# Kernel optimization log

Hardware: AMD Instinct MI355X
Metric: run time of the kernel (lower is better)

Reference implementation:

```python
import jax, jax.numpy as jnp
import numpy as np
import math

B, T, D, H, L, V = 2, 1024, 768, 12, 4, 50257
HD = D // H
ROPE_PCT = 0.5
MAX_WL = 10000.0
EPS = 1e-5


def setup_inputs() -> dict:
    key = jax.random.key(0)
    ks = jax.random.split(key, 8)
    s = 0.02
    return {
        "idx": jax.random.randint(ks[0], (B, T), 0, V, dtype=jnp.int32),
        "wte": jax.random.normal(ks[1], (V, D), jnp.float32) * s,
        "ln1_g": jnp.ones((L, D), jnp.float32),
        "ln1_b": jnp.zeros((L, D), jnp.float32),
        "Wqkv": jax.random.normal(ks[2], (L, D, 3 * D), jnp.float32) * s,
        "bqkv": jnp.zeros((L, 3 * D), jnp.float32),
        "Wo": jax.random.normal(ks[3], (L, D, D), jnp.float32) * s,
        "bo": jnp.zeros((L, D), jnp.float32),
        "ln2_g": jnp.ones((L, D), jnp.float32),
        "ln2_b": jnp.zeros((L, D), jnp.float32),
        "Wfc": jax.random.normal(ks[4], (L, D, 4 * D), jnp.float32) * s,
        "bfc": jnp.zeros((L, 4 * D), jnp.float32),
        "Wp": jax.random.normal(ks[5], (L, 4 * D, D), jnp.float32) * s,
        "bp": jnp.zeros((L, D), jnp.float32),
        "lnf_g": jnp.ones((D,), jnp.float32),
        "lnf_b": jnp.zeros((D,), jnp.float32),
        "Wlm": jax.random.normal(ks[6], (D, V), jnp.float32) * s,
    }


def _ln(x, g, b):
    m = x.mean(-1, keepdims=True)
    v = x.var(-1, keepdims=True)
    return (x - m) / jnp.sqrt(v + EPS) * g + b


def _gelu(x):
    return 0.5 * x * (1.0 + jnp.tanh(math.sqrt(2.0 / math.pi) * (x + 0.044715 * x ** 3)))


def _p_rope(x, positions):
    # x: [B, H, T, HD]; partial RoPE: rotate first ROPE_PCT of angle pairs, leave rest.
    rope_angles = int(ROPE_PCT * HD // 2)
    nope_angles = HD // 2 - rope_angles
    fraction = 2.0 * jnp.arange(0, rope_angles) / HD
    timescale = jnp.power(MAX_WL, fraction)
    timescale = jnp.pad(timescale, (0, nope_angles), constant_values=jnp.inf)
    sinusoid = positions[:, None] / timescale[None, :]  # [T, HD//2]; pos/inf = 0 -> no rotation
    sin, cos = jnp.sin(sinusoid), jnp.cos(sinusoid)
    first, second = jnp.split(x, 2, axis=-1)
    out = jnp.concatenate([first * cos - second * sin, second * cos + first * sin], axis=-1)
    return out.astype(x.dtype)


def reference(idx, wte, ln1_g, ln1_b, Wqkv, bqkv, Wo, bo, ln2_g, ln2_b, Wfc, bfc, Wp, bp, lnf_g, lnf_b, Wlm):
    x = wte[idx]  # [B, T, D]
    positions = jnp.arange(T, dtype=x.dtype)
    causal = jnp.tril(jnp.ones((T, T), dtype=bool))
    scale = jnp.sqrt(jnp.float32(HD)).astype(x.dtype)
    for l in range(L):
        h1 = _ln(x, ln1_g[l], ln1_b[l])
        h2 = _ln(x, ln2_g[l], ln2_b[l])  # note: both LNs read the same x (as in source)
        # attention
        qkv = h1 @ Wqkv[l] + bqkv[l]
        q, k, v = jnp.split(qkv, 3, axis=-1)
        sh = lambda t: t.reshape(B, T, H, HD).transpose(0, 2, 1, 3)
        q, k, v = sh(q), sh(k), sh(v)
        q = _p_rope(q, positions)
        k = _p_rope(k, positions)
        att = jnp.einsum('bhqd,bhkd->bhqk', q, k) / scale
        att = jnp.where(causal, att, jnp.finfo(att.dtype).min)
        att = jax.nn.softmax(att, axis=-1)
        y = jnp.einsum('bhqk,bhkd->bhqd', att, v)
        y = y.transpose(0, 2, 1, 3).reshape(B, T, D)
        x = x + (y @ Wo[l] + bo[l])
        # MLP
        h = _gelu(h2 @ Wfc[l] + bfc[l])
        x = x + (h @ Wp[l] + bp[l])
    x = _ln(x, lnf_g, lnf_b)
    logits = x @ Wlm  # [B, T, V]
    return logits
```

## Files before the change

### kernel.cpp

```cpp
#include <hip/hip_runtime.h>

typedef unsigned short u16;
typedef unsigned int u32;
typedef __attribute__((ext_vector_type(8))) short bf16x8;
typedef __attribute__((ext_vector_type(4))) float f32x4;

#define SEQ 1024
#define DM 768
#define NH 12
#define HD2 64
#define NLAYER 4
#define NVOCAB 50257
#define BT 2048

__device__ __forceinline__ u16 f2bf(float f) {
  union { float f; u32 u; } v; v.f = f;
  u32 r = v.u + 0x7FFFu + ((v.u >> 16) & 1u);
  return (u16)(r >> 16);
}
__device__ __forceinline__ float bf2f(u16 u) {
  union { u32 u; float f; } v; v.u = ((u32)u) << 16;
  return v.f;
}

__device__ __forceinline__ void glds16(const u16* g, u16* l) {
  __builtin_amdgcn_global_load_lds(
      (const __attribute__((address_space(1))) u32*)(const void*)g,
      (__attribute__((address_space(3))) u32*)(void*)l, 16, 0, 0);
}

__global__ void k_embed(const int* __restrict__ idx, const float* __restrict__ wte,
                        float* __restrict__ xf) {
  int r = blockIdx.x;
  int tok = idx[r];
  const float* s = wte + (size_t)tok * DM;
  float* d = xf + (size_t)r * DM;
  for (int c = threadIdx.x; c < DM; c += 256) d[c] = s[c];
}

__global__ void k_trig(float* __restrict__ ctab, float* __restrict__ stab) {
  int gid = blockIdx.x * 256 + threadIdx.x;
  int tt = gid >> 4, j = gid & 15;
  float inv = powf(10000.f, -(float)j * (1.f / 32.f));
  float ang = (float)tt * inv;
  ctab[gid] = cosf(ang);
  stab[gid] = sinf(ang);
}

__global__ void k_cvtT(const float* __restrict__ in, u16* __restrict__ out,
                       int R, int C) {
  __shared__ u16 t[64][68];
  int c0 = blockIdx.x * 64, r0 = blockIdx.y * 64;
  int tx = threadIdx.x & 15, ty = threadIdx.x >> 4;
  int c = c0 + tx * 4;
#pragma unroll
  for (int i = 0; i < 4; ++i) {
    int r = r0 + ty + i * 16;
    float4 v = make_float4(0.f, 0.f, 0.f, 0.f);
    if (c + 3 < C) {
      v = *(const float4*)&in[(size_t)r * C + c];
    } else {
      if (c + 0 < C) v.x = in[(size_t)r * C + c];
      if (c + 1 < C) v.y = in[(size_t)r * C + c + 1];
      if (c + 2 < C) v.z = in[(size_t)r * C + c + 2];
      if (c + 3 < C) v.w = in[(size_t)r * C + c + 3];
    }
    t[ty + i * 16][tx * 4 + 0] = f2bf(v.x);
    t[ty + i * 16][tx * 4 + 1] = f2bf(v.y);
    t[ty + i * 16][tx * 4 + 2] = f2bf(v.z);
    t[ty + i * 16][tx * 4 + 3] = f2bf(v.w);
  }
  __syncthreads();
  int wl = threadIdx.x & 31, grp = threadIdx.x >> 5;
#pragma unroll
  for (int it = 0; it < 8; ++it) {
    int cc = it * 8 + grp;
    int gcol = c0 + cc;
    if (gcol < C) {
      u32 wv = (u32)t[2 * wl][cc] | ((u32)t[2 * wl + 1][cc] << 16);
      *(u32*)&out[(size_t)gcol * R + r0 + 2 * wl] = wv;
    }
  }
}

__device__ __forceinline__ float bsum(float v, float* red) {
#pragma unroll
  for (int o = 32; o > 0; o >>= 1) v += __shfl_down(v, o);
  if ((threadIdx.x & 63) == 0) red[threadIdx.x >> 6] = v;
  __syncthreads();
  if (threadIdx.x == 0) red[4] = red[0] + red[1] + red[2] + red[3];
  __syncthreads();
  return red[4];
}

__global__ void k_ln(const float* __restrict__ x, const float* __restrict__ g1,
                     const float* __restrict__ b1, const float* __restrict__ g2,
                     const float* __restrict__ b2, u16* __restrict__ o1,
                     u16* __restrict__ o2) {
  __shared__ float red[8];
  int r = blockIdx.x;
  int t = threadIdx.x;
  const float* xr = x + (size_t)r * DM;
  float v0 = xr[t], v1 = xr[t + 256], v2 = xr[t + 512];
  float mean = bsum(v0 + v1 + v2, red) * (1.f / DM);
  float d0 = v0 - mean, d1 = v1 - mean, d2 = v2 - mean;
  float var = bsum(d0 * d0 + d1 * d1 + d2 * d2, red) * (1.f / DM);
  float rstd = rsqrtf(var + 1e-5f);
  u16* p1 = o1 + (size_t)r * DM;
  p1[t]       = f2bf(d0 * rstd * g1[t]       + b1[t]);
  p1[t + 256] = f2bf(d1 * rstd * g1[t + 256] + b1[t + 256]);
  p1[t + 512] = f2bf(d2 * rstd * g1[t + 512] + b1[t + 512]);
  if (o2) {
    u16* p2 = o2 + (size_t)r * DM;
    p2[t]       = f2bf(d0 * rstd * g2[t]       + b2[t]);
    p2[t + 256] = f2bf(d1 * rstd * g2[t + 256] + b2[t + 256]);
    p2[t + 512] = f2bf(d2 * rstd * g2[t + 512] + b2[t + 512]);
  }
}

__global__ void k_attn(const u16* __restrict__ qr, const u16* __restrict__ kr,
                       const u16* __restrict__ vT, u16* __restrict__ yb) {
  int ti = (int)gridDim.x - 1 - (int)blockIdx.x;
  int bh = blockIdx.y;
  __shared__ u16 Ps[64 * 72];
  __shared__ u16 Ks[2][4096];
  __shared__ u16 Vs[2][4096];
  int tid = threadIdx.x;
  int rr = tid >> 2, cc = tid & 3;
  int w = tid >> 6, l = tid & 63;
  int rl = l & 15, g = l >> 4;
  {
    const u16* gq = qr + ((size_t)bh * SEQ + ti * 64 + rr) * HD2;
    *(uint4*)&Ps[rr * 72 + cc * 8]      = *(const uint4*)(gq + cc * 8);
    *(uint4*)&Ps[rr * 72 + cc * 8 + 32] = *(const uint4*)(gq + cc * 8 + 32);
  }
  int srow = w * 8 + (l >> 3);
  int gs = (l & 7) ^ (l >> 3);
  const u16* gkb = kr + (size_t)bh * SEQ * HD2;
  const u16* gvb = vT + (size_t)bh * HD2 * SEQ;
  glds16(gkb + (size_t)srow * 64 + gs * 8,        &Ks[0][w * 512]);
  glds16(gkb + (size_t)(32 + srow) * 64 + gs * 8, &Ks[0][2048 + w * 512]);
  glds16(gvb + (size_t)srow * SEQ + gs * 8,       &Vs[0][w * 512]);
  glds16(gvb + (size_t)(32 + srow) * SEQ + gs * 8,&Vs[0][2048 + w * 512]);
  __syncthreads();
  bf16x8 aq0 = *(const bf16x8*)&Ps[(w * 16 + rl) * 72 + g * 8];
  bf16x8 aq1 = *(const bf16x8*)&Ps[(w * 16 + rl) * 72 + 32 + g * 8];
  float m[4], lsum[4];
  f32x4 oacc[4] = {};
#pragma unroll
  for (int r2 = 0; r2 < 4; ++r2) { m[r2] = -3.0e38f; lsum[r2] = 0.f; }
  int qloc = w * 16 + g * 4;
  int sw = rl & 7;
  int cur = 0;
  for (int kt = 0; kt <= ti; ++kt) {
    if (kt < ti) {
      int nx = cur ^ 1;
      glds16(gkb + (size_t)((kt + 1) * 64 + srow) * 64 + gs * 8,      &Ks[nx][w * 512]);
      glds16(gkb + (size_t)((kt + 1) * 64 + 32 + srow) * 64 + gs * 8, &Ks[nx][2048 + w * 512]);
      glds16(gvb + (size_t)srow * SEQ + (kt + 1) * 64 + gs * 8,       &Vs[nx][w * 512]);
      glds16(gvb + (size_t)(32 + srow) * SEQ + (kt + 1) * 64 + gs * 8,&Vs[nx][2048 + w * 512]);
    }
    f32x4 s[4] = {};
    __builtin_amdgcn_s_setprio(1);
#pragma unroll
    for (int nt = 0; nt < 4; ++nt) {
      int r = (nt * 16 + rl) * 64;
      bf16x8 b0 = *(const bf16x8*)&Ks[cur][r + ((0 + g) ^ sw) * 8];
      bf16x8 b1 = *(const bf16x8*)&Ks[cur][r + ((4 + g) ^ sw) * 8];
      s[nt] = __builtin_amdgcn_mfma_f32_16x16x32_bf16(aq0, b0, s[nt], 0, 0, 0);
      s[nt] = __builtin_amdgcn_mfma_f32_16x16x32_bf16(aq1, b1, s[nt], 0, 0, 0);
    }
    __builtin_amdgcn_s_setprio(0);
#pragma unroll
    for (int nt = 0; nt < 4; ++nt) s[nt] *= 0.125f;
    if (kt == ti) {
#pragma unroll
      for (int nt = 0; nt < 4; ++nt) {
        int col = nt * 16 + rl;
#pragma unroll
        for (int r2 = 0; r2 < 4; ++r2)
          if (col > qloc + r2) s[nt][r2] = -3.0e38f;
      }
    }
#pragma unroll
    for (int r2 = 0; r2 < 4; ++r2) {
      float pm = fmaxf(fmaxf(s[0][r2], s[1][r2]), fmaxf(s[2][r2], s[3][r2]));
#pragma unroll
      for (int o = 1; o < 16; o <<= 1) pm = fmaxf(pm, __shfl_xor(pm, o));
      float mn = fmaxf(m[r2], pm);
      float corr = __expf(m[r2] - mn);
      float p0 = __expf(s[0][r2] - mn);
      float p1 = __expf(s[1][r2] - mn);
      float p2 = __expf(s[2][r2] - mn);
      float p3 = __expf(s[3][r2] - mn);
      float ps = p0 + p1 + p2 + p3;
#pragma unroll
      for (int o = 1; o < 16; o <<= 1) ps += __shfl_xor(ps, o);
      lsum[r2] = lsum[r2] * corr + ps;
      m[r2] = mn;
      oacc[0][r2] *= corr; oacc[1][r2] *= corr;
      oacc[2][r2] *= corr; oacc[3][r2] *= corr;
      int prow = (qloc + r2) * 72;
      Ps[prow + rl]      = f2bf(p0);
      Ps[prow + 16 + rl] = f2bf(p1);
      Ps[prow + 32 + rl] = f2bf(p2);
      Ps[prow + 48 + rl] = f2bf(p3);
    }
    bf16x8 pa0 = *(const bf16x8*)&Ps[(w * 16 + rl) * 72 + g * 8];
    bf16x8 pa1 = *(const bf16x8*)&Ps[(w * 16 + rl) * 72 + 32 + g * 8];
    __builtin_amdgcn_s_setprio(1);
#pragma unroll
    for (int nt = 0; nt < 4; ++nt) {
      int r = (nt * 16 + rl) * 64;
      bf16x8 b0 = *(const bf16x8*)&Vs[cur][r + ((0 + g) ^ sw) * 8];
      bf16x8 b1 = *(const bf16x8*)&Vs[cur][r + ((4 + g) ^ sw) * 8];
      oacc[nt] = __builtin_amdgcn_mfma_f32_16x16x32_bf16(pa0, b0, oacc[nt], 0, 0, 0);
      oacc[nt] = __builtin_amdgcn_mfma_f32_16x16x32_bf16(pa1, b1, oacc[nt], 0, 0, 0);
    }
    __builtin_amdgcn_s_setprio(0);
    __syncthreads();
    cur ^= 1;
  }
  int b = bh / NH, h = bh % NH;
  float invl[4];
#pragma unroll
  for (int r2 = 0; r2 < 4; ++r2) invl[r2] = 1.f / lsum[r2];
#pragma unroll
  for (int nt = 0; nt < 4; ++nt) {
    int d = nt * 16 + rl;
#pragma unroll
    for (int r2 = 0; r2 < 4; ++r2) {
      int trow = ti * 64 + qloc + r2;
      yb[((size_t)(b * SEQ + trow)) * DM + h * HD2 + d] = f2bf(oacc[nt][r2] * invl[r2]);
    }
  }
}

template <int MODE>
__global__ void k_g128(const u16* __restrict__ A, const u16* __restrict__ Bt,
                       const float* __restrict__ bias, u16* __restrict__ outb,
                       float* __restrict__ outf, int M, int N, int K, int MT,
                       const float* __restrict__ ctab,
                       const float* __restrict__ stab, u16* __restrict__ qrp,
                       u16* __restrict__ krp, u16* __restrict__ vTp) {
  __shared__ u16 SM[16384];
  float* cw = (float*)SM;
  int nwg = gridDim.x;
  int id = blockIdx.x;
  if ((nwg & 7) == 0) id = (id & 7) * (nwg >> 3) + (id >> 3);
  int mt = id % MT, nt = id / MT;
  int m0 = mt * 128, n0 = nt * 128;
  int tid = threadIdx.x;
  int w = tid >> 6, l = tid & 63;
  int srow = w * 16 + (l >> 2);
  int gs = (l & 3) ^ ((l >> 3) & 3);
  const u16* gA0 = A + (size_t)(m0 + srow) * K + gs * 8;
  const u16* gA1 = A + (size_t)(m0 + 64 + srow) * K + gs * 8;
  int rb0 = n0 + srow;      if (rb0 > N - 1) rb0 = N - 1;
  int rb1 = n0 + 64 + srow; if (rb1 > N - 1) rb1 = N - 1;
  const u16* gB0 = Bt + (size_t)rb0 * K + gs * 8;
  const u16* gB1 = Bt + (size_t)rb1 * K + gs * 8;
  int wm = (w >> 1) * 64, wn = (w & 1) * 64;
  int rl = l & 15, g = l >> 4;
  int sla = g ^ ((rl >> 1) & 3);
  f32x4 acc[4][4] = {};
  int nK = K >> 5;
  int cur = 0;
  {
    u16* dA = SM + w * 512;
    glds16(gA0, dA); glds16(gA1, dA + 2048);
    u16* dB = SM + 4096 + w * 512;
    glds16(gB0, dB); glds16(gB1, dB + 2048);
  }
  __syncthreads();
  for (int kt = 0; kt < nK; ++kt) {
    if (kt + 1 < nK) {
      u16* dA = SM + (cur ^ 1) * 8192 + w * 512;
      glds16(gA0 + (kt + 1) * 32, dA); glds16(gA1 + (kt + 1) * 32, dA + 2048);
      u16* dB = dA + 4096;
      glds16(gB0 + (kt + 1) * 32, dB); glds16(gB1 + (kt + 1) * 32, dB + 2048);
    }
    const u16* As = SM + cur * 8192;
    const u16* Bs = As + 4096;
    bf16x8 af[4], bfr[4];
    __builtin_amdgcn_s_setprio(1);
#pragma unroll
    for (int i = 0; i < 4; ++i)
      af[i] = *(const bf16x8*)&As[(wm + i * 16 + rl) * 32 + sla * 8];
#pragma unroll
    for (int j = 0; j < 4; ++j)
      bfr[j] = *(const bf16x8*)&Bs[(wn + j * 16 + rl) * 32 + sla * 8];
#pragma unroll
    for (int i = 0; i < 4; ++i)
#pragma unroll
      for (int j = 0; j < 4; ++j)
        acc[i][j] = __builtin_amdgcn_mfma_f32_16x16x32_bf16(af[i], bfr[j],
                                                            acc[i][j], 0, 0, 0);
    __builtin_amdgcn_s_setprio(0);
    __syncthreads();
    cur ^= 1;
  }
  int reg = n0 / DM;
  int h0 = (n0 % DM) / 64;
  int bb = m0 >> 10;
  int t0 = m0 & (SEQ - 1);
  size_t bhbase = (size_t)bb * NH;
#pragma unroll
  for (int ch = 0; ch < 4; ++ch) {
    if ((w >> 1) == (ch >> 1)) {
      int ib = (ch & 1) * 2;
#pragma unroll
      for (int ii = 0; ii < 2; ++ii) {
#pragma unroll
        for (int j = 0; j < 4; ++j) {
          int col = wn + j * 16 + rl;
#pragma unroll
          for (int r2 = 0; r2 < 4; ++r2) {
            int rowc = ii * 16 + g * 4 + r2;
            float v = acc[ib + ii][j][r2];
            if (MODE != 3) {
              v += bias[n0 + col];
              if (MODE == 1) {
                float u = 0.7978845608028654f * (v + 0.044715f * v * v * v);
                v = 0.5f * v * (1.f + tanhf(u));
              }
            }
            cw[rowc * 132 + col] = v;
          }
        }
      }
    }
    __syncthreads();
    if (MODE == 3) {
      for (int t = tid; t < 4096; t += 256) {
        int rowc = t >> 7, col = t & 127;
        int gc = n0 + col;
        if (gc < N)
          __builtin_nontemporal_store(cw[rowc * 132 + col],
                                      &outf[(size_t)(m0 + ch * 32 + rowc) * N + gc]);
      }
    } else if (MODE == 1) {
      for (int t = tid; t < 2048; t += 256) {
        int rowc = t >> 6, cp = t & 63;
        u32 wv = (u32)f2bf(cw[rowc * 132 + 2 * cp]) |
                 ((u32)f2bf(cw[rowc * 132 + 2 * cp + 1]) << 16);
        *(u32*)&outb[(size_t)(m0 + ch * 32 + rowc) * N + n0 + 2 * cp] = wv;
      }
    } else {
      if (reg < 2) {
        u16* dst = (reg == 0) ? qrp : krp;
        for (int t = tid; t < 2048; t += 256) {
          int rowc = t >> 6, cp = t & 63;
          int c = 2 * cp;
          int hh = c >> 6, d = c & 63;
          int tt = t0 + ch * 32 + rowc;
          float x0 = cw[rowc * 132 + c];
          float x1 = cw[rowc * 132 + c + 1];
          float o0, o1;
          if (d < 32) {
            float y0 = cw[rowc * 132 + c + 32];
            float y1 = cw[rowc * 132 + c + 33];
            float c0 = 1.f, s0 = 0.f, c1 = 1.f, s1 = 0.f;
            if (d < 16) {
              c0 = ctab[tt * 16 + d];     s0 = stab[tt * 16 + d];
              c1 = ctab[tt * 16 + d + 1]; s1 = stab[tt * 16 + d + 1];
            }
            o0 = x0 * c0 - y0 * s0;
            o1 = x1 * c1 - y1 * s1;
          } else {
            int j = d - 32;
            float y0 = cw[rowc * 132 + c - 32];
            float y1 = cw[rowc * 132 + c - 31];
            float c0 = 1.f, s0 = 0.f, c1 = 1.f, s1 = 0.f;
            if (j < 16) {
              c0 = ctab[tt * 16 + j];     s0 = stab[tt * 16 + j];
              c1 = ctab[tt * 16 + j + 1]; s1 = stab[tt * 16 + j + 1];
            }
            o0 = x0 * c0 + y0 * s0;
            o1 = x1 * c1 + y1 * s1;
          }
          u32 wv = (u32)f2bf(o0) | ((u32)f2bf(o1) << 16);
          *(u32*)&dst[((bhbase + h0 + hh) * SEQ + tt) * HD2 + d] = wv;
        }
      } else {
        for (int t = tid; t < 2048; t += 256) {
          int dcol = t >> 4, p = t & 15;
          int hh = dcol >> 6, d = dcol & 63;
          int tt = t0 + ch * 32 + 2 * p;
          u32 wv = (u32)f2bf(cw[(2 * p) * 132 + dcol]) |
                   ((u32)f2bf(cw[(2 * p + 1) * 132 + dcol]) << 16);
          *(u32*)&vTp[((bhbase + h0 + hh) * HD2 + d) * SEQ + tt] = wv;
        }
      }
    }
    __syncthreads();
  }
}

__global__ void k_gemm64(const u16* __restrict__ A, const u16* __restrict__ Bt,
                         const float* __restrict__ bias,
                         float* __restrict__ outf, int M, int N, int K, int MT) {
  __shared__ u16 As[8192];
  __shared__ u16 Bs[8192];
  int nwg = gridDim.x;
  int id = blockIdx.x;
  if ((nwg & 7) == 0) id = (id & 7) * (nwg >> 3) + (id >> 3);
  int mt = id % MT, nt = id / MT;
  int sk = blockIdx.y, nsk = gridDim.y;
  int Kc = K / nsk, k0 = sk * Kc;
  int m0 = mt * 64, n0 = nt * 64;
  int tid = threadIdx.x;
  int w = tid >> 6, l = tid & 63;
  int row0 = tid >> 3, slot0 = tid & 7;
  int gs0 = slot0 ^ (row0 & 7);
  const u16* gA0 = A + (size_t)(m0 + row0) * K + k0 + gs0 * 8;
  const u16* gA1 = gA0 + (size_t)32 * K;
  const u16* gB0 = Bt + (size_t)(n0 + row0) * K + k0 + gs0 * 8;
  const u16* gB1 = gB0 + (size_t)32 * K;
  int wm = (w >> 1) * 32, wn = (w & 1) * 32;
  int rl = l & 15, g = l >> 4;
  int sl0 = g ^ (rl & 7), sl1 = (4 + g) ^ (rl & 7);
  f32x4 acc[2][2] = {};
  int nK = Kc >> 6;
  int cur = 0;
  {
    glds16(gA0, As + w * 512); glds16(gA1, As + 2048 + w * 512);
    glds16(gB0, Bs + w * 512); glds16(gB1, Bs + 2048 + w * 512);
  }
  __syncthreads();
  for (int kt = 0; kt < nK; ++kt) {
    if (kt + 1 < nK) {
      int nx = (cur ^ 1) * 4096;
      glds16(gA0 + (kt + 1) * 64, As + nx + w * 512);
      glds16(gA1 + (kt + 1) * 64, As + nx + 2048 + w * 512);
      glds16(gB0 + (kt + 1) * 64, Bs + nx + w * 512);
      glds16(gB1 + (kt + 1) * 64, Bs + nx + 2048 + w * 512);
    }
    const u16* Ac = As + cur * 4096;
    const u16* Bc = Bs + cur * 4096;
    bf16x8 a0[2], a1[2], b0[2], b1[2];
    __builtin_amdgcn_s_setprio(1);
#pragma unroll
    for (int i = 0; i < 2; ++i) {
      int r = (wm + i * 16 + rl) * 64;
      a0[i] = *(const bf16x8*)&Ac[r + sl0 * 8];
      a1[i] = *(const bf16x8*)&Ac[r + sl1 * 8];
    }
#pragma unroll
    for (int j = 0; j < 2; ++j) {
      int r = (wn + j * 16 + rl) * 64;
      b0[j] = *(const bf16x8*)&Bc[r + sl0 * 8];
      b1[j] = *(const bf16x8*)&Bc[r + sl1 * 8];
    }
#pragma unroll
    for (int i = 0; i < 2; ++i)
#pragma unroll
      for (int j = 0; j < 2; ++j) {
        acc[i][j] = __builtin_amdgcn_mfma_f32_16x16x32_bf16(a0[i], b0[j],
                                                            acc[i][j], 0, 0, 0);
        acc[i][j] = __builtin_amdgcn_mfma_f32_16x16x32_bf16(a1[i], b1[j],
                                                            acc[i][j], 0, 0, 0);
      }
    __builtin_amdgcn_s_setprio(0);
    __syncthreads();
    cur ^= 1;
  }
#pragma unroll
  for (int i = 0; i < 2; ++i) {
#pragma unroll
    for (int j = 0; j < 2; ++j) {
      int col = n0 + wn + j * 16 + rl;
      float bv = bias ? bias[col] : 0.f;
#pragma unroll
      for (int r2 = 0; r2 < 4; ++r2) {
        int row = m0 + wm + i * 16 + g * 4 + r2;
        float v = acc[i][j][r2];
        if (sk == 0) v += bv;
        atomicAdd(&outf[(size_t)row * N + col], v);
      }
    }
  }
}

__global__ void k_gemm_f32b(const u16* __restrict__ A, const float* __restrict__ B,
                            float* __restrict__ outf, int M, int N, int K) {
  __shared__ u16 As[128 * 40];
  __shared__ u16 Bs[4 * 128 * 12];
  int tid = threadIdx.x;
  int wid = tid >> 6, lane = tid & 63;
  int rl = lane & 15, g = lane >> 4;
  int m0 = blockIdx.x * 128, n0 = blockIdx.y * 128;
  int wm = (wid >> 1) * 64, wn = (wid & 1) * 64;
  int ar = tid >> 2, ac = tid & 3;
  int bn = tid & 127, bq = tid >> 7;
  f32x4 acc[4][4] = {};
  int nK = K / 32;
  for (int kt = 0; kt < nK; ++kt) {
    __syncthreads();
    {
      const u16* ga = A + (size_t)(m0 + ar) * K + kt * 32 + ac * 8;
      *(uint4*)&As[ar * 40 + ac * 8] = *(const uint4*)ga;
      *(uint4*)&As[(ar + 64) * 40 + ac * 8] = *(const uint4*)(ga + (size_t)64 * K);
    }
    int col = n0 + bn;
#pragma unroll
    for (int r = 0; r < 4; ++r) {
      int kq = bq + 2 * r;
      int kk = kt * 32 + kq * 4;
      float f0 = 0.f, f1 = 0.f, f2v = 0.f, f3 = 0.f;
      if (col < N) {
        const float* gb = B + (size_t)kk * N + col;
        f0 = gb[0]; f1 = gb[(size_t)N]; f2v = gb[(size_t)2 * N]; f3 = gb[(size_t)3 * N];
      }
      uint2 wv;
      wv.x = (u32)f2bf(f0) | ((u32)f2bf(f1) << 16);
      wv.y = (u32)f2bf(f2v) | ((u32)f2bf(f3) << 16);
      *(uint2*)&Bs[(kq >> 1) * 1536 + bn * 12 + (kq & 1) * 4] = wv;
    }
    __syncthreads();
    bf16x8 af[4], bfr[4];
#pragma unroll
    for (int mt = 0; mt < 4; ++mt)
      af[mt] = *(const bf16x8*)&As[(wm + mt * 16 + rl) * 40 + g * 8];
#pragma unroll
    for (int nt = 0; nt < 4; ++nt) {
      const u16* p = &Bs[g * 1536 + (wn + nt * 16 + rl) * 12];
      union { bf16x8 v; uint2 u2[2]; } tmp;
      tmp.u2[0] = *(const uint2*)p;
      tmp.u2[1] = *(const uint2*)(p + 4);
      bfr[nt] = tmp.v;
    }
#pragma unroll
    for (int mt = 0; mt < 4; ++mt)
#pragma unroll
      for (int nt = 0; nt < 4; ++nt)
        acc[mt][nt] = __builtin_amdgcn_mfma_f32_16x16x32_bf16(af[mt], bfr[nt],
                                                              acc[mt][nt], 0, 0, 0);
  }
#pragma unroll
  for (int mt = 0; mt < 4; ++mt)
#pragma unroll
    for (int nt = 0; nt < 4; ++nt) {
      int col = n0 + wn + nt * 16 + rl;
      if (col >= N) continue;
#pragma unroll
      for (int r2 = 0; r2 < 4; ++r2) {
        int row = m0 + wm + mt * 16 + g * 4 + r2;
        outf[(size_t)row * N + col] = acc[mt][nt][r2];
      }
    }
}

extern "C" void kernel_launch(void* const* d_in, const int* in_sizes, int n_in,
                              void* d_out, int out_size, void* d_ws, size_t ws_size,
                              hipStream_t stream) {
  (void)in_sizes; (void)n_in; (void)out_size;
  const int*   idx  = (const int*)  d_in[0];
  const float* wte  = (const float*)d_in[1];
  const float* ln1g = (const float*)d_in[2];
  const float* ln1b = (const float*)d_in[3];
  const float* Wqkv = (const float*)d_in[4];
  const float* bqkv = (const float*)d_in[5];
  const float* Wo   = (const float*)d_in[6];
  const float* bo   = (const float*)d_in[7];
  const float* ln2g = (const float*)d_in[8];
  const float* ln2b = (const float*)d_in[9];
  const float* Wfc  = (const float*)d_in[10];
  const float* bfc  = (const float*)d_in[11];
  const float* Wp   = (const float*)d_in[12];
  const float* bp   = (const float*)d_in[13];
  const float* lnfg = (const float*)d_in[14];
  const float* lnfb = (const float*)d_in[15];
  const float* Wlm  = (const float*)d_in[16];
  float* out = (float*)d_out;

  char* sb = (char*)d_out;
  size_t off = 0;
  auto alloc = [&](size_t bytes) {
    char* p = sb + off;
    off += (bytes + 255) & ~(size_t)255;
    return (void*)p;
  };
  float* xf  = (float*)alloc((size_t)BT * DM * 4);
  u16* h1b   = (u16*)alloc((size_t)BT * DM * 2);
  u16* h2b   = (u16*)alloc((size_t)BT * DM * 2);
  u16* qr    = (u16*)alloc((size_t)BT * DM * 2);
  u16* kr    = (u16*)alloc((size_t)BT * DM * 2);
  u16* vT    = (u16*)alloc((size_t)BT * DM * 2);
  u16* yb    = (u16*)alloc((size_t)BT * DM * 2);
  u16* hgel  = (u16*)alloc((size_t)BT * 4 * DM * 2);
  float* ctab = (float*)alloc((size_t)SEQ * 16 * 4);
  float* stab = (float*)alloc((size_t)SEQ * 16 * 4);
  u16* wqkvT = (u16*)alloc((size_t)NLAYER * 3 * DM * DM * 2);
  u16* woT   = (u16*)alloc((size_t)NLAYER * DM * DM * 2);
  u16* wfcT  = (u16*)alloc((size_t)NLAYER * 4 * DM * DM * 2);
  u16* wpT   = (u16*)alloc((size_t)NLAYER * 4 * DM * DM * 2);

  size_t wlmT_bytes = (size_t)NVOCAB * DM * 2;
  size_t xlnf_bytes = (size_t)BT * DM * 2;
  bool fast_lm = ws_size >= wlmT_bytes + xlnf_bytes + 512;
  u16* wlmT = (u16*)d_ws;
  u16* xlnf = fast_lm ? (u16*)((char*)d_ws + ((wlmT_bytes + 255) & ~(size_t)255))
                      : (u16*)d_ws;

  k_trig<<<(SEQ * 16) / 256, 256, 0, stream>>>(ctab, stab);
  for (int l = 0; l < NLAYER; ++l) {
    k_cvtT<<<dim3((3 * DM + 63) / 64, DM / 64), 256, 0, stream>>>(
        Wqkv + (size_t)l * DM * 3 * DM, wqkvT + (size_t)l * 3 * DM * DM, DM, 3 * DM);
    k_cvtT<<<dim3(DM / 64, DM / 64), 256, 0, stream>>>(
        Wo + (size_t)l * DM * DM, woT + (size_t)l * DM * DM, DM, DM);
    k_cvtT<<<dim3((4 * DM) / 64, DM / 64), 256, 0, stream>>>(
        Wfc + (size_t)l * DM * 4 * DM, wfcT + (size_t)l * 4 * DM * DM, DM, 4 * DM);
    k_cvtT<<<dim3(DM / 64, (4 * DM) / 64), 256, 0, stream>>>(
        Wp + (size_t)l * 4 * DM * DM, wpT + (size_t)l * 4 * DM * DM, 4 * DM, DM);
  }
  if (fast_lm)
    k_cvtT<<<dim3((NVOCAB + 63) / 64, DM / 64), 256, 0, stream>>>(Wlm, wlmT, DM, NVOCAB);

  k_embed<<<BT, 256, 0, stream>>>(idx, wte, xf);
  for (int l = 0; l < NLAYER; ++l) {
    k_ln<<<BT, 256, 0, stream>>>(xf, ln1g + l * DM, ln1b + l * DM,
                                 ln2g + l * DM, ln2b + l * DM, h1b, h2b);
    k_g128<4><<<(BT / 128) * (3 * DM / 128), 256, 0, stream>>>(
        h1b, wqkvT + (size_t)l * 3 * DM * DM, bqkv + (size_t)l * 3 * DM,
        nullptr, nullptr, BT, 3 * DM, DM, BT / 128, ctab, stab, qr, kr, vT);
    k_attn<<<dim3(SEQ / 64, 2 * NH), 256, 0, stream>>>(qr, kr, vT, yb);
    k_gemm64<<<dim3((BT / 64) * (DM / 64), 2), 256, 0, stream>>>(
        yb, woT + (size_t)l * DM * DM, bo + (size_t)l * DM, xf, BT, DM, DM, BT / 64);
    k_g128<1><<<(BT / 128) * (4 * DM / 128), 256, 0, stream>>>(
        h2b, wfcT + (size_t)l * 4 * DM * DM, bfc + (size_t)l * 4 * DM,
        hgel, nullptr, BT, 4 * DM, DM, BT / 128,
        nullptr, nullptr, nullptr, nullptr, nullptr);
    k_gemm64<<<dim3((BT / 64) * (DM / 64), 4), 256, 0, stream>>>(
        hgel, wpT + (size_t)l * 4 * DM * DM, bp + (size_t)l * DM, xf, BT, DM, 4 * DM,
        BT / 64);
  }
  k_ln<<<BT, 256, 0, stream>>>(xf, lnfg, lnfb, nullptr, nullptr, xlnf, nullptr);
  if (fast_lm) {
    int nt = (NVOCAB + 127) / 128;
    k_g128<3><<<(BT / 128) * nt, 256, 0, stream>>>(
        xlnf, wlmT, nullptr, nullptr, out, BT, NVOCAB, DM, BT / 128,
        nullptr, nullptr, nullptr, nullptr, nullptr);
  } else {
    k_gemm_f32b<<<dim3(BT / 128, (NVOCAB + 127) / 128), 256, 0, stream>>>(
        xlnf, Wlm, out, BT, NVOCAB, DM);
  }
}
```

Before: 1.057 ms.

## Add 64x128 GEMM kernel for QKV/FC, fold softmax scale into Q, lazy rescale

The QKV and FC projections move to a new 64x128-tile kernel with a BK=64 double-buffered LDS pipeline, giving twice as many workgroups, and k_g128 is cut down to the LM-head path only. The 1/sqrt(d) softmax scale is folded into Q during the RoPE epilogue, removing the per-tile multiply in attention. Attention also switches to a lazy max-rescale that only rescales the accumulators when the row max grows by more than 8, skipping many exp and multiply ops. The lazy threshold lets unnormalised probabilities reach about e^8, which stays safe in fp32 but slightly changes bf16 rounding of P.

```diff
diff --git a/kernel.cpp b/kernel.cpp
--- a/kernel.cpp
+++ b/kernel.cpp
@@ -171,8 +171,6 @@
       s[nt] = __builtin_amdgcn_mfma_f32_16x16x32_bf16(aq1, b1, s[nt], 0, 0, 0);
     }
     __builtin_amdgcn_s_setprio(0);
-#pragma unroll
-    for (int nt = 0; nt < 4; ++nt) s[nt] *= 0.125f;
     if (kt == ti) {
 #pragma unroll
       for (int nt = 0; nt < 4; ++nt) {
@@ -187,19 +185,21 @@
       float pm = fmaxf(fmaxf(s[0][r2], s[1][r2]), fmaxf(s[2][r2], s[3][r2]));
 #pragma unroll
       for (int o = 1; o < 16; o <<= 1) pm = fmaxf(pm, __shfl_xor(pm, o));
-      float mn = fmaxf(m[r2], pm);
-      float corr = __expf(m[r2] - mn);
-      float p0 = __expf(s[0][r2] - mn);
-      float p1 = __expf(s[1][r2] - mn);
-      float p2 = __expf(s[2][r2] - mn);
-      float p3 = __expf(s[3][r2] - mn);
+      if (pm > m[r2] + 8.f) {
+        float corr = __expf(m[r2] - pm);
+        m[r2] = pm;
+        lsum[r2] *= corr;
+        oacc[0][r2] *= corr; oacc[1][r2] *= corr;
+        oacc[2][r2] *= corr; oacc[3][r2] *= corr;
+      }
+      float p0 = __expf(s[0][r2] - m[r2]);
+      float p1 = __expf(s[1][r2] - m[r2]);
+      float p2 = __expf(s[2][r2] - m[r2]);
+      float p3 = __expf(s[3][r2] - m[r2]);
       float ps = p0 + p1 + p2 + p3;
 #pragma unroll
       for (int o = 1; o < 16; o <<= 1) ps += __shfl_xor(ps, o);
-      lsum[r2] = lsum[r2] * corr + ps;
-      m[r2] = mn;
-      oacc[0][r2] *= corr; oacc[1][r2] *= corr;
-      oacc[2][r2] *= corr; oacc[3][r2] *= corr;
+      lsum[r2] += ps;
       int prow = (qloc + r2) * 72;
       Ps[prow + rl]      = f2bf(p0);
       Ps[prow + 16 + rl] = f2bf(p1);
@@ -238,11 +238,7 @@
 
 template <int MODE>
 __global__ void k_g128(const u16* __restrict__ A, const u16* __restrict__ Bt,
-                       const float* __restrict__ bias, u16* __restrict__ outb,
-                       float* __restrict__ outf, int M, int N, int K, int MT,
-                       const float* __restrict__ ctab,
-                       const float* __restrict__ stab, u16* __restrict__ qrp,
-                       u16* __restrict__ krp, u16* __restrict__ vTp) {
+                       float* __restrict__ outf, int M, int N, int K, int MT) {
   __shared__ u16 SM[16384];
   float* cw = (float*)SM;
   int nwg = gridDim.x;
@@ -300,11 +296,6 @@
     __syncthreads();
     cur ^= 1;
   }
-  int reg = n0 / DM;
-  int h0 = (n0 % DM) / 64;
-  int bb = m0 >> 10;
-  int t0 = m0 & (SEQ - 1);
-  size_t bhbase = (size_t)bb * NH;
 #pragma unroll
   for (int ch = 0; ch < 4; ++ch) {
     if ((w >> 1) == (ch >> 1)) {
@@ -317,89 +308,182 @@
 #pragma unroll
           for (int r2 = 0; r2 < 4; ++r2) {
             int rowc = ii * 16 + g * 4 + r2;
-            float v = acc[ib + ii][j][r2];
-            if (MODE != 3) {
-              v += bias[n0 + col];
-              if (MODE == 1) {
-                float u = 0.7978845608028654f * (v + 0.044715f * v * v * v);
-                v = 0.5f * v * (1.f + tanhf(u));
-              }
-            }
-            cw[rowc * 132 + col] = v;
+            cw[rowc * 132 + col] = acc[ib + ii][j][r2];
           }
         }
       }
     }
     __syncthreads();
-    if (MODE == 3) {
+    for (int t = tid; t < 4096; t += 256) {
+      int rowc = t >> 7, col = t & 127;
+      int gc = n0 + col;
+      if (gc < N)
+        __builtin_nontemporal_store(cw[rowc * 132 + col],
+                                    &outf[(size_t)(m0 + ch * 32 + rowc) * N + gc]);
+    }
+    __syncthreads();
+  }
+}
+
+template <int MODE>
+__global__ void k_gw(const u16* __restrict__ A, const u16* __restrict__ Bt,
+                     const float* __restrict__ bias, u16* __restrict__ outb,
+                     int M, int N, int K, int MT,
+                     const float* __restrict__ ctab,
+                     const float* __restrict__ stab, u16* __restrict__ qrp,
+                     u16* __restrict__ krp, u16* __restrict__ vTp) {
+  __shared__ u16 SM2[24576];
+  float* cw = (float*)SM2;
+  int nwg = gridDim.x;
+  int id = blockIdx.x;
+  if ((nwg & 7) == 0) id = (id & 7) * (nwg >> 3) + (id >> 3);
+  int mt = id % MT, nt = id / MT;
+  int m0 = mt * 64, n0 = nt * 128;
+  int tid = threadIdx.x;
+  int w = tid >> 6, l = tid & 63;
+  int row0 = tid >> 3, slot0 = tid & 7;
+  int gs0 = slot0 ^ (row0 & 7);
+  const u16* gA0 = A + (size_t)(m0 + row0) * K + gs0 * 8;
+  const u16* gA1 = gA0 + (size_t)32 * K;
+  const u16* gB0 = Bt + (size_t)(n0 + row0) * K + gs0 * 8;
+  const u16* gB1 = gB0 + (size_t)32 * K;
+  const u16* gB2 = gB0 + (size_t)64 * K;
+  const u16* gB3 = gB0 + (size_t)96 * K;
+  int wm = (w >> 1) * 32, wn = (w & 1) * 64;
+  int rl = l & 15, g = l >> 4;
+  int sl0 = g ^ (rl & 7), sl1 = (4 + g) ^ (rl & 7);
+  f32x4 acc[2][4] = {};
+  int nK = K >> 6;
+  int cur = 0;
+  {
+    u16* dA = SM2;
+    glds16(gA0, dA + w * 512); glds16(gA1, dA + 2048 + w * 512);
+    u16* dB = SM2 + 8192;
+    glds16(gB0, dB + w * 512);        glds16(gB1, dB + 2048 + w * 512);
+    glds16(gB2, dB + 4096 + w * 512); glds16(gB3, dB + 6144 + w * 512);
+  }
+  __syncthreads();
+  for (int kt = 0; kt < nK; ++kt) {
+    if (kt + 1 < nK) {
+      int ka = (kt + 1) * 64;
+      u16* dA = SM2 + (cur ^ 1) * 4096;
+      glds16(gA0 + ka, dA + w * 512); glds16(gA1 + ka, dA + 2048 + w * 512);
+      u16* dB = SM2 + 8192 + (cur ^ 1) * 8192;
+      glds16(gB0 + ka, dB + w * 512);        glds16(gB1 + ka, dB + 2048 + w * 512);
+      glds16(gB2 + ka, dB + 4096 + w * 512); glds16(gB3 + ka, dB + 6144 + w * 512);
+    }
+    const u16* Ac = SM2 + cur * 4096;
+    const u16* Bc = SM2 + 8192 + cur * 8192;
+    bf16x8 a0[2], a1[2], b0[4], b1[4];
+    __builtin_amdgcn_s_setprio(1);
+#pragma unroll
+    for (int i = 0; i < 2; ++i) {
+      int r = (wm + i * 16 + rl) * 64;
+      a0[i] = *(const bf16x8*)&Ac[r + sl0 * 8];
+      a1[i] = *(const bf16x8*)&Ac[r + sl1 * 8];
+    }
+#pragma unroll
+    for (int j = 0; j < 4; ++j) {
+      int r = (wn + j * 16 + rl) * 64;
+      b0[j] = *(const bf16x8*)&Bc[r + sl0 * 8];
+      b1[j] = *(const bf16x8*)&Bc[r + sl1 * 8];
+    }
+#pragma unroll
+    for (int i = 0; i < 2; ++i)
+#pragma unroll
+      for (int j = 0; j < 4; ++j) {
+        acc[i][j] = __builtin_amdgcn_mfma_f32_16x16x32_bf16(a0[i], b0[j],
+                                                            acc[i][j], 0, 0, 0);
+        acc[i][j] = __builtin_amdgcn_mfma_f32_16x16x32_bf16(a1[i], b1[j],
+                                                            acc[i][j], 0, 0, 0);
+      }
+    __builtin_amdgcn_s_setprio(0);
+    __syncthreads();
+    cur ^= 1;
+  }
+#pragma unroll
+  for (int i = 0; i < 2; ++i) {
+#pragma unroll
+    for (int j = 0; j < 4; ++j) {
+      int col = wn + j * 16 + rl;
+      float bv = bias[n0 + col];
+#pragma unroll
+      for (int r2 = 0; r2 < 4; ++r2) {
+        float v = acc[i][j][r2] + bv;
+        if (MODE == 1) {
+          float u = 0.7978845608028654f * (v + 0.044715f * v * v * v);
+          v = 0.5f * v * (1.f + tanhf(u));
+        }
+        cw[(wm + i * 16 + g * 4 + r2) * 133 + col] = v;
+      }
+    }
+  }
+  __syncthreads();
+  if (MODE == 1) {
+    for (int t = tid; t < 4096; t += 256) {
+      int rowc = t >> 6, cp = t & 63;
+      u32 wv = (u32)f2bf(cw[rowc * 133 + 2 * cp]) |
+               ((u32)f2bf(cw[rowc * 133 + 2 * cp + 1]) << 16);
+      *(u32*)&outb[(size_t)(m0 + rowc) * N + n0 + 2 * cp] = wv;
+    }
+  } else {
+    int reg = n0 / DM;
+    int h0 = (n0 % DM) / 64;
+    int bb = m0 >> 10;
+    int t0 = m0 & (SEQ - 1);
+    size_t bhb = (size_t)bb * NH + h0;
+    if (reg < 2) {
+      u16* dst = (reg == 0) ? qrp : krp;
+      float qs = (reg == 0) ? 0.125f : 1.f;
       for (int t = tid; t < 4096; t += 256) {
-        int rowc = t >> 7, col = t & 127;
-        int gc = n0 + col;
-        if (gc < N)
-          __builtin_nontemporal_store(cw[rowc * 132 + col],
-                                      &outf[(size_t)(m0 + ch * 32 + rowc) * N + gc]);
-      }
-    } else if (MODE == 1) {
-      for (int t = tid; t < 2048; t += 256) {
         int rowc = t >> 6, cp = t & 63;
-        u32 wv = (u32)f2bf(cw[rowc * 132 + 2 * cp]) |
-                 ((u32)f2bf(cw[rowc * 132 + 2 * cp + 1]) << 16);
-        *(u32*)&outb[(size_t)(m0 + ch * 32 + rowc) * N + n0 + 2 * cp] = wv;
+        int c = 2 * cp;
+        int hh = c >> 6, d = c & 63;
+        int tt = t0 + rowc;
+        float x0 = cw[rowc * 133 + c];
+        float x1 = cw[rowc * 133 + c + 1];
+        float o0, o1;
+        if (d < 32) {
+          float y0 = cw[rowc * 133 + c + 32];
+          float y1 = cw[rowc * 133 + c + 33];
+          float c0 = 1.f, s0 = 0.f, c1 = 1.f, s1 = 0.f;
+          if (d < 16) {
+            c0 = ctab[tt * 16 + d];     s0 = stab[tt * 16 + d];
+            c1 = ctab[tt * 16 + d + 1]; s1 = stab[tt * 16 + d + 1];
+          }
+          o0 = x0 * c0 - y0 * s0;
+          o1 = x1 * c1 - y1 * s1;
+        } else {
+          int j = d - 32;
+          float y0 = cw[rowc * 133 + c - 32];
+          float y1 = cw[rowc * 133 + c - 31];
+          float c0 = 1.f, s0 = 0.f, c1 = 1.f, s1 = 0.f;
+          if (j < 16) {
+            c0 = ctab[tt * 16 + j];     s0 = stab[tt * 16 + j];
+            c1 = ctab[tt * 16 + j + 1]; s1 = stab[tt * 16 + j + 1];
+          }
+          o0 = x0 * c0 + y0 * s0;
+          o1 = x1 * c1 + y1 * s1;
+        }
+        u32 wv = (u32)f2bf(o0 * qs) | ((u32)f2bf(o1 * qs) << 16);
+        *(u32*)&dst[((bhb + hh) * SEQ + tt) * HD2 + d] = wv;
       }
     } else {
-      if (reg < 2) {
-        u16* dst = (reg == 0) ? qrp : krp;
-        for (int t = tid; t < 2048; t += 256) {
-          int rowc = t >> 6, cp = t & 63;
-          int c = 2 * cp;
-          int hh = c >> 6, d = c & 63;
-          int tt = t0 + ch * 32 + rowc;
-          float x0 = cw[rowc * 132 + c];
-          float x1 = cw[rowc * 132 + c + 1];
-          float o0, o1;
-          if (d < 32) {
-            float y0 = cw[rowc * 132 + c + 32];
-            float y1 = cw[rowc * 132 + c + 33];
-            float c0 = 1.f, s0 = 0.f, c1 = 1.f, s1 = 0.f;
-            if (d < 16) {
-              c0 = ctab[tt * 16 + d];     s0 = stab[tt * 16 + d];
-              c1 = ctab[tt * 16 + d + 1]; s1 = stab[tt * 16 + d + 1];
-            }
-            o0 = x0 * c0 - y0 * s0;
-            o1 = x1 * c1 - y1 * s1;
-          } else {
-            int j = d - 32;
-            float y0 = cw[rowc * 132 + c - 32];
-            float y1 = cw[rowc * 132 + c - 31];
-            float c0 = 1.f, s0 = 0.f, c1 = 1.f, s1 = 0.f;
-            if (j < 16) {
-              c0 = ctab[tt * 16 + j];     s0 = stab[tt * 16 + j];
-              c1 = ctab[tt * 16 + j + 1]; s1 = stab[tt * 16 + j + 1];
-            }
-            o0 = x0 * c0 + y0 * s0;
-            o1 = x1 * c1 + y1 * s1;
-          }
-          u32 wv = (u32)f2bf(o0) | ((u32)f2bf(o1) << 16);
-          *(u32*)&dst[((bhbase + h0 + hh) * SEQ + tt) * HD2 + d] = wv;
-        }
-      } else {
-        for (int t = tid; t < 2048; t += 256) {
-          int dcol = t >> 4, p = t & 15;
-          int hh = dcol >> 6, d = dcol & 63;
-          int tt = t0 + ch * 32 + 2 * p;
-          u32 wv = (u32)f2bf(cw[(2 * p) * 132 + dcol]) |
-                   ((u32)f2bf(cw[(2 * p + 1) * 132 + dcol]) << 16);
-          *(u32*)&vTp[((bhbase + h0 + hh) * HD2 + d) * SEQ + tt] = wv;
-        }
-      }
-    }
-    __syncthreads();
-  }
-}
-
-__global__ void k_gemm64(const u16* __restrict__ A, const u16* __restrict__ Bt,
-                         const float* __restrict__ bias,
-                         float* __restrict__ outf, int M, int N, int K, int MT) {
+      for (int t = tid; t < 4096; t += 256) {
+        int dcol = t >> 5, p = t & 31;
+        int hh = dcol >> 6, d = dcol & 63;
+        int tt = t0 + 2 * p;
+        u32 wv = (u32)f2bf(cw[(2 * p) * 133 + dcol]) |
+                 ((u32)f2bf(cw[(2 * p + 1) * 133 + dcol]) << 16);
+        *(u32*)&vTp[((bhb + hh) * HD2 + d) * SEQ + tt] = wv;
+      }
+    }
+  }
+}
+
+__global__ void k_g64r(const u16* __restrict__ A, const u16* __restrict__ Bt,
+                       const float* __restrict__ bias,
+                       float* __restrict__ outf, int M, int N, int K, int MT) {
   __shared__ u16 As[8192];
   __shared__ u16 Bs[8192];
   int nwg = gridDim.x;
@@ -621,17 +705,16 @@
   for (int l = 0; l < NLAYER; ++l) {
     k_ln<<<BT, 256, 0, stream>>>(xf, ln1g + l * DM, ln1b + l * DM,
                                  ln2g + l * DM, ln2b + l * DM, h1b, h2b);
-    k_g128<4><<<(BT / 128) * (3 * DM / 128), 256, 0, stream>>>(
+    k_gw<4><<<(BT / 64) * (3 * DM / 128), 256, 0, stream>>>(
         h1b, wqkvT + (size_t)l * 3 * DM * DM, bqkv + (size_t)l * 3 * DM,
-        nullptr, nullptr, BT, 3 * DM, DM, BT / 128, ctab, stab, qr, kr, vT);
+        nullptr, BT, 3 * DM, DM, BT / 64, ctab, stab, qr, kr, vT);
     k_attn<<<dim3(SEQ / 64, 2 * NH), 256, 0, stream>>>(qr, kr, vT, yb);
-    k_gemm64<<<dim3((BT / 64) * (DM / 64), 2), 256, 0, stream>>>(
+    k_g64r<<<dim3((BT / 64) * (DM / 64), 2), 256, 0, stream>>>(
         yb, woT + (size_t)l * DM * DM, bo + (size_t)l * DM, xf, BT, DM, DM, BT / 64);
-    k_g128<1><<<(BT / 128) * (4 * DM / 128), 256, 0, stream>>>(
+    k_gw<1><<<(BT / 64) * (4 * DM / 128), 256, 0, stream>>>(
         h2b, wfcT + (size_t)l * 4 * DM * DM, bfc + (size_t)l * 4 * DM,
-        hgel, nullptr, BT, 4 * DM, DM, BT / 128,
-        nullptr, nullptr, nullptr, nullptr, nullptr);
-    k_gemm64<<<dim3((BT / 64) * (DM / 64), 4), 256, 0, stream>>>(
+        hgel, BT, 4 * DM, DM, BT / 64, nullptr, nullptr, nullptr, nullptr, nullptr);
+    k_g64r<<<dim3((BT / 64) * (DM / 64), 4), 256, 0, stream>>>(
         hgel, wpT + (size_t)l * 4 * DM * DM, bp + (size_t)l * DM, xf, BT, DM, 4 * DM,
         BT / 64);
   }
@@ -639,8 +722,7 @@
   if (fast_lm) {
     int nt = (NVOCAB + 127) / 128;
     k_g128<3><<<(BT / 128) * nt, 256, 0, stream>>>(
-        xlnf, wlmT, nullptr, nullptr, out, BT, NVOCAB, DM, BT / 128,
-        nullptr, nullptr, nullptr, nullptr, nullptr);
+        xlnf, wlmT, out, BT, NVOCAB, DM, BT / 128);
   } else {
     k_gemm_f32b<<<dim3(BT / 128, (NVOCAB + 127) / 128), 256, 0, stream>>>(
         xlnf, Wlm, out, BT, NVOCAB, DM);
```

Result: faster. 963.8 us (-8.8%).
